# Optimization experiments

Measured on AMD Instinct MI355X. Metric: run time of the kernel, lower is better.

## Reference

```python
import jax, jax.numpy as jnp
import numpy as np

EMBED_DIM = 1024
NUM_HEADS = 16
HEAD_DIM = EMBED_DIM // NUM_HEADS


def setup_inputs() -> dict:
    key = jax.random.key(0)
    ks = jax.random.split(key, 5)
    scale = 1.0 / np.sqrt(EMBED_DIM)
    x = jax.random.normal(ks[0], (2, 2048, EMBED_DIM), dtype=jnp.float32)
    W_qkv = jax.random.uniform(ks[1], (EMBED_DIM, 3 * EMBED_DIM), jnp.float32, -scale, scale)
    b_qkv = jax.random.uniform(ks[2], (3 * EMBED_DIM,), jnp.float32, -scale, scale)
    W_out = jax.random.uniform(ks[3], (EMBED_DIM, EMBED_DIM), jnp.float32, -scale, scale)
    b_out = jax.random.uniform(ks[4], (EMBED_DIM,), jnp.float32, -scale, scale)
    return {"x": x, "W_qkv": W_qkv, "b_qkv": b_qkv, "W_out": W_out, "b_out": b_out}


def reference(x, W_qkv, b_qkv, W_out, b_out):
    B, T, C = x.shape
    H, D = NUM_HEADS, HEAD_DIM
    qkv = x @ W_qkv + b_qkv                       # [B,T,3C]
    q, k, v = jnp.split(qkv, 3, axis=-1)
    # [B,T,C] -> [B,H,T,D]
    q = q.reshape(B, T, H, D).transpose(0, 2, 1, 3)
    k = k.reshape(B, T, H, D).transpose(0, 2, 1, 3)
    v = v.reshape(B, T, H, D).transpose(0, 2, 1, 3)
    scores = jnp.einsum('bhqd,bhkd->bhqk', q, k) / np.sqrt(D)
    attn = jax.nn.softmax(scores, axis=-1)
    out = jnp.einsum('bhqk,bhkd->bhqd', attn, v)  # [B,H,T,D]
    out = out.transpose(0, 2, 1, 3).reshape(B, T, C)
    return out @ W_out + b_out
```

## Files before the change

kernel.cpp:

```cpp
#include <hip/hip_runtime.h>
#include <hip/hip_bf16.h>

#define TB 2048
#define CC 1024
#define HH 16
#define DD 64
#define MM 4096
#define N3 3072
#define KVB 128
#define NT (TB / KVB)

typedef __bf16 bf16x8 __attribute__((ext_vector_type(8)));
typedef float f32x4 __attribute__((ext_vector_type(4)));
typedef float f32x16 __attribute__((ext_vector_type(16)));
typedef unsigned short ushort8 __attribute__((ext_vector_type(8)));
typedef unsigned short u16;

#define QSCALE 0.180336880693612f

__device__ __forceinline__ u16 f2b(float f) {
    unsigned int x = __float_as_uint(f);
    x = (x + 0x7fffu + ((x >> 16) & 1u)) >> 16;
    return (u16)x;
}

__device__ __forceinline__ unsigned cvt_pk_bf16(float lo, float hi) {
    unsigned r;
    asm("v_cvt_pk_bf16_f32 %0, %1, %2" : "=v"(r) : "v"(lo), "v"(hi));
    return r;
}

__device__ __forceinline__ void gld16(const u16* g, u16* l) {
    __builtin_amdgcn_global_load_lds(
        (const __attribute__((address_space(1))) unsigned int*)g,
        (__attribute__((address_space(3))) unsigned int*)l, 16, 0, 0);
}

__global__ __launch_bounds__(256) void prep(const float* __restrict__ x,
                                            u16* __restrict__ xb,
                                            const float* __restrict__ wqkv,
                                            u16* __restrict__ wqkvT,
                                            const float* __restrict__ wout,
                                            u16* __restrict__ woutT) {
    __shared__ float tl[64][65];
    const int bx = blockIdx.x;
    const int tid = threadIdx.x;
    if (bx < 4096) {
        int i = (bx * 256 + tid) * 4;
        float4 v = *reinterpret_cast<const float4*>(x + i);
        union { u16 u[4]; uint2 v2; } r;
        r.u[0] = f2b(v.x); r.u[1] = f2b(v.y); r.u[2] = f2b(v.z); r.u[3] = f2b(v.w);
        *reinterpret_cast<uint2*>(xb + i) = r.v2;
        return;
    }
    const int idx = bx - 4096;
    const int nb = idx & 63, kb = idx >> 6;
    const float* in; u16* out; int N, n0;
    if (nb < 48) { in = wqkv; out = wqkvT; N = 3072; n0 = nb * 64; }
    else         { in = wout; out = woutT; N = 1024; n0 = (nb - 48) * 64; }
    const int k0 = kb * 64;
#pragma unroll
    for (int rep = 0; rep < 4; ++rep) {
        int r = rep * 16 + (tid >> 4);
        int c4 = (tid & 15) * 4;
        float4 v = *reinterpret_cast<const float4*>(&in[(size_t)(k0 + r) * N + n0 + c4]);
        tl[r][c4] = v.x; tl[r][c4 + 1] = v.y; tl[r][c4 + 2] = v.z; tl[r][c4 + 3] = v.w;
    }
    __syncthreads();
#pragma unroll
    for (int rep = 0; rep < 4; ++rep) {
        int nn = rep * 16 + (tid >> 4);
        int kk4 = (tid & 15) * 4;
        union { u16 u[4]; unsigned long long ll; } pk;
#pragma unroll
        for (int i = 0; i < 4; ++i)
            pk.u[i] = f2b(tl[kk4 + i][nn]);
        *reinterpret_cast<unsigned long long*>(&out[(size_t)(n0 + nn) * 1024 + k0 + kk4]) = pk.ll;
    }
}

__global__ __launch_bounds__(512, 2) void gemm_qkv(const u16* __restrict__ xb,
                                                   const u16* __restrict__ wT,
                                                   const float* __restrict__ bias,
                                                   u16* __restrict__ qg,
                                                   u16* __restrict__ kg,
                                                   u16* __restrict__ vtg) {
    __shared__ u16 smem[65536];
    u16* const A0 = smem;
    u16* const B0 = smem + 16384;
    u16* const A1 = smem + 32768;
    u16* const B1 = smem + 49152;
    const int id = blockIdx.y * 12 + blockIdx.x;
    const int xcd = id & 7, pos = id >> 3;
    const int m0 = ((xcd >> 1) * 4 + pos / 6) * 256;
    const int n0 = ((xcd & 1) * 6 + pos % 6) * 256;
    const int tid = threadIdx.x;
    const int w = tid >> 6, lane = tid & 63, lr = lane & 15, h = lane >> 4;
    const int wr = w >> 2, wc = w & 3;
    f32x4 acc[8][4] = {};
    bf16x8 bB[4][2];
    bf16x8 a[2][2];

#define STAGE_SIDE(dstb, srcp, rowbase, kt) do {                                      \
    _Pragma("unroll")                                                                 \
    for (int jj = 0; jj < 4; ++jj) {                                                  \
        int L = jj * 512 + tid;                                                       \
        int rr = L >> 3, c8 = L & 7;                                                  \
        gld16((srcp) + (size_t)((rowbase) + rr) * 1024 + (kt) * 64                    \
                  + ((c8 ^ (rr & 7)) << 3),                                           \
              (dstb) + L * 8);                                                        \
    } } while (0)
#define DSREAD_B(PB) do {                                                             \
    _Pragma("unroll")                                                                 \
    for (int n = 0; n < 4; ++n) {                                                     \
        int R = wc * 64 + n * 16 + lr;                                                \
        const char* br = (const char*)(PB) + R * 128;                                 \
        bB[n][0] = *reinterpret_cast<const bf16x8*>(br + ((h ^ (R & 7)) << 4));       \
        bB[n][1] = *reinterpret_cast<const bf16x8*>(br + (((4 + h) ^ (R & 7)) << 4)); \
    } } while (0)
#define DSREAD_A(PA, mb) do {                                                         \
    _Pragma("unroll")                                                                 \
    for (int mi = 0; mi < 2; ++mi) {                                                  \
        int R = wr * 128 + ((mb) + mi) * 16 + lr;                                     \
        const char* ar = (const char*)(PA) + R * 128;                                 \
        a[mi][0] = *reinterpret_cast<const bf16x8*>(ar + ((h ^ (R & 7)) << 4));       \
        a[mi][1] = *reinterpret_cast<const bf16x8*>(ar + (((4 + h) ^ (R & 7)) << 4)); \
    } } while (0)
#define MFMAP(mb) do {                                                                \
    _Pragma("unroll")                                                                 \
    for (int mi = 0; mi < 2; ++mi)                                                    \
        _Pragma("unroll")                                                             \
        for (int n = 0; n < 4; ++n) {                                                 \
            acc[(mb) + mi][n] = __builtin_amdgcn_mfma_f32_16x16x32_bf16(              \
                a[mi][0], bB[n][0], acc[(mb) + mi][n], 0, 0, 0);                      \
            acc[(mb) + mi][n] = __builtin_amdgcn_mfma_f32_16x16x32_bf16(              \
                a[mi][1], bB[n][1], acc[(mb) + mi][n], 0, 0, 0);                      \
        } } while (0)
#define GBAR __builtin_amdgcn_s_barrier()
#define VMC(n) asm volatile("s_waitcnt vmcnt(" #n ")" ::: "memory")
#define LGK0 do { asm volatile("s_waitcnt lgkmcnt(0)" ::: "memory");                  \
                  __builtin_amdgcn_sched_barrier(0); } while (0)
#define PRI1 __builtin_amdgcn_s_setprio(1)
#define PRI0 __builtin_amdgcn_s_setprio(0)

    STAGE_SIDE(A0, xb, m0, 0);
    STAGE_SIDE(B0, wT, n0, 0);

#pragma unroll 1
    for (int i = 0; i < 7; ++i) {
        const int t1 = 2 * i + 1, t2 = 2 * i + 2;
        STAGE_SIDE(A1, xb, m0, t1);
        VMC(4); GBAR;
        DSREAD_B(B0); DSREAD_A(A0, 0); LGK0;
        PRI1; MFMAP(0); PRI0; GBAR;
        STAGE_SIDE(B1, wT, n0, t1);
        DSREAD_A(A0, 2); GBAR; LGK0; PRI1; MFMAP(2); PRI0; GBAR;
        DSREAD_A(A0, 4); GBAR; LGK0; PRI1; MFMAP(4); PRI0; GBAR;
        DSREAD_A(A0, 6); GBAR; LGK0; PRI1; MFMAP(6); PRI0; GBAR;
        STAGE_SIDE(A0, xb, m0, t2);
        VMC(4); GBAR;
        DSREAD_B(B1); DSREAD_A(A1, 0); LGK0;
        PRI1; MFMAP(0); PRI0; GBAR;
        STAGE_SIDE(B0, wT, n0, t2);
        DSREAD_A(A1, 2); GBAR; LGK0; PRI1; MFMAP(2); PRI0; GBAR;
        DSREAD_A(A1, 4); GBAR; LGK0; PRI1; MFMAP(4); PRI0; GBAR;
        DSREAD_A(A1, 6); GBAR; LGK0; PRI1; MFMAP(6); PRI0; GBAR;
    }
    STAGE_SIDE(A1, xb, m0, 15);
    VMC(4); GBAR;
    DSREAD_B(B0); DSREAD_A(A0, 0); LGK0;
    PRI1; MFMAP(0); PRI0; GBAR;
    STAGE_SIDE(B1, wT, n0, 15);
    DSREAD_A(A0, 2); GBAR; LGK0; PRI1; MFMAP(2); PRI0; GBAR;
    DSREAD_A(A0, 4); GBAR; LGK0; PRI1; MFMAP(4); PRI0; GBAR;
    DSREAD_A(A0, 6); GBAR; LGK0; PRI1; MFMAP(6); PRI0; GBAR;
    VMC(0); GBAR;
    DSREAD_B(B1); DSREAD_A(A1, 0); LGK0;
    PRI1; MFMAP(0); PRI0; GBAR;
    DSREAD_A(A1, 2); GBAR; LGK0; PRI1; MFMAP(2); PRI0; GBAR;
    DSREAD_A(A1, 4); GBAR; LGK0; PRI1; MFMAP(4); PRI0; GBAR;
    DSREAD_A(A1, 6); GBAR; LGK0; PRI1; MFMAP(6); PRI0; GBAR;

#undef STAGE_SIDE
#undef DSREAD_B
#undef DSREAD_A
#undef MFMAP
#undef GBAR
#undef VMC
#undef LGK0
#undef PRI1
#undef PRI0

    const int nthird = n0 >> 10;
    const int b = m0 >> 11, t0 = m0 & 2047;
    float bv[4];
#pragma unroll
    for (int n = 0; n < 4; ++n)
        bv[n] = bias[n0 + wc * 64 + n * 16 + lr];

    __syncthreads();
    if (nthird == 2) {
#pragma unroll
        for (int n = 0; n < 4; ++n) {
            int nloc = wc * 64 + n * 16 + lr;
#pragma unroll
            for (int m = 0; m < 8; ++m) {
                int mloc = wr * 128 + m * 16 + h * 4;
                int mpb = (mloc & ~15) | ((mloc & 4) << 1) | ((mloc & 8) >> 1);
                union { u16 u[4]; unsigned long long ll; } pk4;
#pragma unroll
                for (int reg = 0; reg < 4; ++reg)
                    pk4.u[reg] = f2b(acc[m][n][reg] + bv[n]);
                int slot = mpb >> 3;
                *reinterpret_cast<unsigned long long*>(
                    (char*)smem + nloc * 512 + (((slot ^ (nloc & 31)) << 4) | ((mpb & 7) * 2))) = pk4.ll;
            }
        }
        __syncthreads();
#pragma unroll
        for (int pass = 0; pass < 16; ++pass) {
            int cid = pass * 512 + tid;
            int r = cid >> 5, p = cid & 31;
            ushort8 vch = *reinterpret_cast<const ushort8*>((const char*)smem + r * 512 + (p << 4));
            int tb = p ^ (r & 31);
            int c1 = (n0 & 1023) + r;
            int hh = c1 >> 6, dd = c1 & 63;
            *reinterpret_cast<ushort8*>(
                vtg + ((size_t)(b * HH + hh) * DD + dd) * TB + t0 + tb * 8) = vch;
        }
    } else {
        const float qs = (nthird == 0) ? QSCALE : 1.0f;
#pragma unroll
        for (int m = 0; m < 8; ++m) {
            int rb = wr * 128 + m * 16 + h * 4;
#pragma unroll
            for (int n = 0; n < 4; ++n) {
                int c = wc * 64 + n * 16 + lr;
#pragma unroll
                for (int reg = 0; reg < 4; ++reg) {
                    int r = rb + reg;
                    *reinterpret_cast<u16*>((char*)smem + r * 512 +
                        ((((c >> 3) ^ (r & 31)) << 4) | ((c & 7) << 1)))
                        = f2b((acc[m][n][reg] + bv[n]) * qs);
                }
            }
        }
        __syncthreads();
        u16* dst = (nthird == 0) ? qg : kg;
#pragma unroll
        for (int pass = 0; pass < 16; ++pass) {
            int cid = pass * 512 + tid;
            int r = cid >> 5, p = cid & 31;
            ushort8 vch = *reinterpret_cast<const ushort8*>((const char*)smem + r * 512 + (p << 4));
            int cb = p ^ (r & 31);
            int c1 = (n0 & 1023) + cb * 8;
            int hh = c1 >> 6, dd = c1 & 63;
            *reinterpret_cast<ushort8*>(
                dst + ((size_t)(b * HH + hh) * TB + t0 + r) * DD + dd) = vch;
        }
    }
}

__global__ __launch_bounds__(256, 2) void attn(const u16* __restrict__ qg,
                                               const u16* __restrict__ kg,
                                               const u16* __restrict__ vtg,
                                               u16* __restrict__ ao) {
    __shared__ u16 Kt[2][KVB * 64];
    __shared__ u16 Vt[2][64 * KVB];
    const int bh = blockIdx.x;
    const int q0 = blockIdx.y * 128;
    const int tid = threadIdx.x, w = tid >> 6, lane = tid & 63;
    const int ln = lane & 31, H = lane >> 5;
    const u16* qb = qg + (size_t)bh * TB * DD;
    const u16* kb = kg + (size_t)bh * TB * DD;
    const u16* vb = vtg + (size_t)bh * DD * TB;

#define STAGE(buf, kp, vp) do {                                                         \
    _Pragma("unroll")                                                                   \
    for (int j = 0; j < 4; ++j) {                                                       \
        int L = j * 256 + tid;                                                          \
        int rk = L >> 3, ck = L & 7;                                                    \
        gld16((kp) + (size_t)rk * DD + ((ck ^ (rk & 7)) << 3), Kt[buf] + L * 8);        \
        int rv = L >> 4, cv = L & 15;                                                   \
        gld16((vp) + (size_t)rv * TB + ((cv ^ (rv & 15)) << 3), Vt[buf] + L * 8);       \
    } } while (0)

    bf16x8 bq[4];
#pragma unroll
    for (int dc = 0; dc < 4; ++dc)
        bq[dc] = *reinterpret_cast<const bf16x8*>(
            qb + (size_t)(q0 + w * 32 + ln) * DD + dc * 16 + H * 8);

    f32x16 o[2] = {};
    float m_r = -1e30f;
    float l_r = 0.f;
    f32x16 zero16 = {};

    auto tile_body = [&](const u16* ktc, const u16* vtc) {
        f32x16 s[4];
        __builtin_amdgcn_s_setprio(1);
#pragma unroll
        for (int kb4 = 0; kb4 < 4; ++kb4) {
            int R = kb4 * 32 + ln;
            const char* krow = (const char*)ktc + R * 128;
#pragma unroll
            for (int dc = 0; dc < 4; ++dc) {
                bf16x8 ak = *reinterpret_cast<const bf16x8*>(
                    krow + (((dc * 2 + H) ^ (R & 7)) << 4));
                s[kb4] = __builtin_amdgcn_mfma_f32_32x32x16_bf16(
                    ak, bq[dc], dc == 0 ? zero16 : s[kb4], 0, 0, 0);
            }
        }
        __builtin_amdgcn_s_setprio(0);

        float pm = s[0][0];
#pragma unroll
        for (int kb4 = 0; kb4 < 4; ++kb4) {
            float t0 = fmaxf(fmaxf(s[kb4][0], s[kb4][1]), fmaxf(s[kb4][2], s[kb4][3]));
            float t1 = fmaxf(fmaxf(s[kb4][4], s[kb4][5]), fmaxf(s[kb4][6], s[kb4][7]));
            float t2 = fmaxf(fmaxf(s[kb4][8], s[kb4][9]), fmaxf(s[kb4][10], s[kb4][11]));
            float t3 = fmaxf(fmaxf(s[kb4][12], s[kb4][13]), fmaxf(s[kb4][14], s[kb4][15]));
            pm = fmaxf(pm, fmaxf(fmaxf(t0, t1), fmaxf(t2, t3)));
        }
        pm = fmaxf(pm, __shfl_xor(pm, 32));

        if (!__all(pm - m_r <= 8.0f)) {
            float mn = fmaxf(m_r, pm);
            float fr = __builtin_amdgcn_exp2f(m_r - mn);
            m_r = mn;
            l_r *= fr;
#pragma unroll
            for (int ngd = 0; ngd < 2; ++ngd)
#pragma unroll
                for (int r = 0; r < 16; ++r)
                    o[ngd][r] *= fr;
        }

        float sum = 0.f;
#pragma unroll
        for (int kb4 = 0; kb4 < 4; ++kb4) {
            float ps = 0.f;
#pragma unroll
            for (int r = 0; r < 16; ++r) {
                s[kb4][r] = __builtin_amdgcn_exp2f(s[kb4][r] - m_r);
                ps += s[kb4][r];
            }
            sum += ps;
        }
        sum += __shfl_xor(sum, 32);
        l_r += sum;

        __builtin_amdgcn_s_setprio(1);
#pragma unroll
        for (int kb4 = 0; kb4 < 4; ++kb4) {
#pragma unroll
            for (int b1 = 0; b1 < 2; ++b1) {
                union { unsigned u[4]; bf16x8 v; } ap;
                ap.u[0] = cvt_pk_bf16(s[kb4][8 * b1 + 0], s[kb4][8 * b1 + 1]);
                ap.u[1] = cvt_pk_bf16(s[kb4][8 * b1 + 2], s[kb4][8 * b1 + 3]);
                ap.u[2] = cvt_pk_bf16(s[kb4][8 * b1 + 4], s[kb4][8 * b1 + 5]);
                ap.u[3] = cvt_pk_bf16(s[kb4][8 * b1 + 6], s[kb4][8 * b1 + 7]);
                int c = kb4 * 2 + b1;
#pragma unroll
                for (int ngd = 0; ngd < 2; ++ngd) {
                    int d = ngd * 32 + ln;
                    bf16x8 av = *reinterpret_cast<const bf16x8*>(
                        (const char*)vtc + d * 256 + (((c * 2 + H) ^ (d & 15)) << 4));
                    o[ngd] = __builtin_amdgcn_mfma_f32_32x32x16_bf16(av, ap.v, o[ngd], 0, 0, 0);
                }
            }
        }
        __builtin_amdgcn_s_setprio(0);
    };

    STAGE(0, kb, vb);
    const u16* kp = kb + KVB * DD;
    const u16* vp = vb + KVB;
    __syncthreads();

#pragma unroll 1
    for (int kt2 = 0; kt2 < NT / 2; ++kt2) {
        STAGE(1, kp, vp);
        kp += KVB * DD; vp += KVB;
        tile_body(Kt[0], Vt[0]);
        __syncthreads();
        if (kt2 < NT / 2 - 1) {
            STAGE(0, kp, vp);
            kp += KVB * DD; vp += KVB;
        }
        tile_body(Kt[1], Vt[1]);
        __syncthreads();
    }
#undef STAGE

    const float linv = 1.0f / l_r;
    const int b = bh >> 4, hh = bh & 15;
    const int q = q0 + w * 32 + ln;
    u16* aorow = ao + (size_t)(b * TB + q) * CC + hh * 64;
#pragma unroll
    for (int ngd = 0; ngd < 2; ++ngd) {
#pragma unroll
        for (int rg = 0; rg < 4; ++rg) {
            int dbase = ngd * 32 + 8 * rg + 4 * H;
            union { u16 u[4]; unsigned long long ll; } pk;
#pragma unroll
            for (int r2 = 0; r2 < 4; ++r2)
                pk.u[r2] = f2b(o[ngd][4 * rg + r2] * linv);
            *reinterpret_cast<unsigned long long*>(aorow + dbase) = pk.ll;
        }
    }
}

__global__ __launch_bounds__(256) void gemm_out(const u16* __restrict__ ao,
                                                const u16* __restrict__ wT,
                                                const float* __restrict__ bias,
                                                float* __restrict__ out) {
    __shared__ u16 As[2][64 * 64];
    __shared__ u16 Bs[2][128 * 64];
    const int id = blockIdx.y * 8 + blockIdx.x;
    const int xcd = id & 7, pos = id >> 3;
    const int xr = xcd >> 1, xc = xcd & 1;
    const int pr = pos >> 2, pc = pos & 3;
    const int m0 = (xr * 16 + pr) * 64;
    const int n0 = (xc * 4 + pc) * 128;
    const int tid = threadIdx.x;
    const int w = tid >> 6, lane = tid & 63, lr = lane & 15, h = lane >> 4;
    f32x4 acc[4][2] = {};

#define GO_STAGE(buf, kt) do {                                                        \
    _Pragma("unroll")                                                                 \
    for (int j = 0; j < 2; ++j) {                                                     \
        int L = j * 256 + tid;                                                        \
        int r = L >> 3, c = L & 7;                                                    \
        gld16(ao + (size_t)(m0 + r) * 1024 + (kt) * 64 + ((c ^ (r & 7)) << 3),        \
              As[buf] + L * 8);                                                       \
    }                                                                                 \
    _Pragma("unroll")                                                                 \
    for (int j = 0; j < 4; ++j) {                                                     \
        int L = j * 256 + tid;                                                        \
        int r = L >> 3, c = L & 7;                                                    \
        gld16(wT + (size_t)(n0 + r) * 1024 + (kt) * 64 + ((c ^ (r & 7)) << 3),        \
              Bs[buf] + L * 8);                                                       \
    } } while (0)

    GO_STAGE(0, 0);
    int cur = 0;
#pragma unroll 1
    for (int kt = 0; kt < 16; ++kt) {
        if (kt < 15) {
            GO_STAGE(cur ^ 1, kt + 1);
            asm volatile("s_waitcnt vmcnt(6)" ::: "memory");
        } else {
            asm volatile("s_waitcnt vmcnt(0)" ::: "memory");
        }
        __builtin_amdgcn_s_barrier();
#pragma unroll
        for (int kk = 0; kk < 2; ++kk) {
            bf16x8 a[4], b[2];
            int cc = kk * 4 + h;
#pragma unroll
            for (int m = 0; m < 4; ++m) {
                int R = m * 16 + lr;
                a[m] = *reinterpret_cast<const bf16x8*>((const char*)As[cur] + R * 128 + ((cc ^ (R & 7)) << 4));
            }
#pragma unroll
            for (int n = 0; n < 2; ++n) {
                int R = w * 32 + n * 16 + lr;
                b[n] = *reinterpret_cast<const bf16x8*>((const char*)Bs[cur] + R * 128 + ((cc ^ (R & 7)) << 4));
            }
            __builtin_amdgcn_s_setprio(1);
#pragma unroll
            for (int m = 0; m < 4; ++m)
#pragma unroll
                for (int n = 0; n < 2; ++n)
                    acc[m][n] = __builtin_amdgcn_mfma_f32_16x16x32_bf16(a[m], b[n], acc[m][n], 0, 0, 0);
            __builtin_amdgcn_s_setprio(0);
        }
        __builtin_amdgcn_sched_barrier(0);
        __builtin_amdgcn_s_barrier();
        cur ^= 1;
    }
#undef GO_STAGE

#pragma unroll
    for (int n = 0; n < 2; ++n) {
        int ng = n0 + w * 32 + n * 16 + lr;
        float bv = bias[ng];
#pragma unroll
        for (int m = 0; m < 4; ++m) {
#pragma unroll
            for (int reg = 0; reg < 4; ++reg) {
                int mg = m0 + m * 16 + h * 4 + reg;
                out[(size_t)mg * 1024 + ng] = acc[m][n][reg] + bv;
            }
        }
    }
}

extern "C" void kernel_launch(void* const* d_in, const int* in_sizes, int n_in,
                              void* d_out, int out_size, void* d_ws, size_t ws_size,
                              hipStream_t stream) {
    const float* x     = (const float*)d_in[0];
    const float* W_qkv = (const float*)d_in[1];
    const float* b_qkv = (const float*)d_in[2];
    const float* W_out = (const float*)d_in[3];
    const float* b_out = (const float*)d_in[4];
    float* out = (float*)d_out;

    char* ws = (char*)d_ws;
    u16* xb    = (u16*)(ws);
    u16* wqkvT = (u16*)(ws + (size_t)( 8u << 20));
    u16* woutT = (u16*)(ws + (size_t)(14u << 20));
    u16* qg    = (u16*)(ws + (size_t)(16u << 20));
    u16* kg    = (u16*)(ws + (size_t)(24u << 20));
    u16* vtg   = (u16*)(ws + (size_t)(32u << 20));
    u16* ao    = xb;

    hipLaunchKernelGGL(prep, dim3(5120), dim3(256), 0, stream, x, xb, W_qkv, wqkvT, W_out, woutT);
    hipLaunchKernelGGL(gemm_qkv, dim3(12, 16), dim3(512), 0, stream, xb, wqkvT, b_qkv, qg, kg, vtg);
    hipLaunchKernelGGL(attn, dim3(32, 16), dim3(256), 0, stream, qg, kg, vtg, ao);
    hipLaunchKernelGGL(gemm_out, dim3(8, 64), dim3(256), 0, stream, ao, woutT, b_out, out);
}
```

Before: 110.3 us.

## Software-pipeline attention loop: overlap next tile's QK^T with current softmax+PV

Restructures the attention KV loop so the QK^T MFMAs for tile t+1 are issued before the softmax and PV of tile t, with K and V staged separately at different pipeline offsets. The goal is to let MFMA work overlap with the exp/max VALU work inside one wave and to hide load latency. In exchange it keeps two score accumulators live (sA and sB, 128 extra fp32 registers), which risks spills or lower occupancy under launch_bounds(256,2).

```diff
diff --git a/kernel.cpp b/kernel.cpp
--- a/kernel.cpp
+++ b/kernel.cpp
@@ -275,15 +275,99 @@
     const u16* kb = kg + (size_t)bh * TB * DD;
     const u16* vb = vtg + (size_t)bh * DD * TB;
 
-#define STAGE(buf, kp, vp) do {                                                         \
+#define STAGE_K(buf, kt) do {                                                           \
     _Pragma("unroll")                                                                   \
     for (int j = 0; j < 4; ++j) {                                                       \
         int L = j * 256 + tid;                                                          \
         int rk = L >> 3, ck = L & 7;                                                    \
-        gld16((kp) + (size_t)rk * DD + ((ck ^ (rk & 7)) << 3), Kt[buf] + L * 8);        \
+        gld16(kb + (size_t)((kt) * KVB + rk) * DD + ((ck ^ (rk & 7)) << 3),             \
+              Kt[buf] + L * 8);                                                         \
+    } } while (0)
+#define STAGE_V(buf, kt) do {                                                           \
+    _Pragma("unroll")                                                                   \
+    for (int j = 0; j < 4; ++j) {                                                       \
+        int L = j * 256 + tid;                                                          \
         int rv = L >> 4, cv = L & 15;                                                   \
-        gld16((vp) + (size_t)rv * TB + ((cv ^ (rv & 15)) << 3), Vt[buf] + L * 8);       \
+        gld16(vb + (size_t)rv * TB + (kt) * KVB + ((cv ^ (rv & 15)) << 3),              \
+              Vt[buf] + L * 8);                                                         \
     } } while (0)
+
+#define QK_PHASE(S, KBUF) do {                                                          \
+    const u16* ktc_ = Kt[KBUF];                                                         \
+    __builtin_amdgcn_s_setprio(1);                                                      \
+    _Pragma("unroll")                                                                   \
+    for (int kb4 = 0; kb4 < 4; ++kb4) {                                                 \
+        int R = kb4 * 32 + ln;                                                          \
+        const char* krow = (const char*)ktc_ + R * 128;                                 \
+        _Pragma("unroll")                                                               \
+        for (int dc = 0; dc < 4; ++dc) {                                                \
+            bf16x8 ak = *reinterpret_cast<const bf16x8*>(                               \
+                krow + (((dc * 2 + H) ^ (R & 7)) << 4));                                \
+            S[kb4] = __builtin_amdgcn_mfma_f32_32x32x16_bf16(                           \
+                ak, bq[dc], dc == 0 ? zero16 : S[kb4], 0, 0, 0);                        \
+        }                                                                               \
+    }                                                                                   \
+    __builtin_amdgcn_s_setprio(0);                                                      \
+} while (0)
+
+#define SMPV(S, VBUF) do {                                                              \
+    const u16* vtc_ = Vt[VBUF];                                                         \
+    float pm = S[0][0];                                                                 \
+    _Pragma("unroll")                                                                   \
+    for (int kb4 = 0; kb4 < 4; ++kb4) {                                                 \
+        float t0_ = fmaxf(fmaxf(S[kb4][0], S[kb4][1]), fmaxf(S[kb4][2], S[kb4][3]));    \
+        float t1_ = fmaxf(fmaxf(S[kb4][4], S[kb4][5]), fmaxf(S[kb4][6], S[kb4][7]));    \
+        float t2_ = fmaxf(fmaxf(S[kb4][8], S[kb4][9]), fmaxf(S[kb4][10], S[kb4][11]));  \
+        float t3_ = fmaxf(fmaxf(S[kb4][12], S[kb4][13]), fmaxf(S[kb4][14], S[kb4][15]));\
+        pm = fmaxf(pm, fmaxf(fmaxf(t0_, t1_), fmaxf(t2_, t3_)));                        \
+    }                                                                                   \
+    pm = fmaxf(pm, __shfl_xor(pm, 32));                                                 \
+    if (!__all(pm - m_r <= 8.0f)) {                                                     \
+        float mn = fmaxf(m_r, pm);                                                      \
+        float fr = __builtin_amdgcn_exp2f(m_r - mn);                                    \
+        m_r = mn;                                                                       \
+        l_r *= fr;                                                                      \
+        _Pragma("unroll")                                                               \
+        for (int ngd = 0; ngd < 2; ++ngd)                                               \
+            _Pragma("unroll")                                                           \
+            for (int r = 0; r < 16; ++r)                                                \
+                o[ngd][r] *= fr;                                                        \
+    }                                                                                   \
+    float sum = 0.f;                                                                    \
+    _Pragma("unroll")                                                                   \
+    for (int kb4 = 0; kb4 < 4; ++kb4) {                                                 \
+        float ps = 0.f;                                                                 \
+        _Pragma("unroll")                                                               \
+        for (int r = 0; r < 16; ++r) {                                                  \
+            S[kb4][r] = __builtin_amdgcn_exp2f(S[kb4][r] - m_r);                        \
+            ps += S[kb4][r];                                                            \
+        }                                                                               \
+        sum += ps;                                                                      \
+    }                                                                                   \
+    sum += __shfl_xor(sum, 32);                                                         \
+    l_r += sum;                                                                         \
+    __builtin_amdgcn_s_setprio(1);                                                      \
+    _Pragma("unroll")                                                                   \
+    for (int kb4 = 0; kb4 < 4; ++kb4) {                                                 \
+        _Pragma("unroll")                                                               \
+        for (int b1 = 0; b1 < 2; ++b1) {                                                \
+            union { unsigned u[4]; bf16x8 v; } ap;                                      \
+            ap.u[0] = cvt_pk_bf16(S[kb4][8 * b1 + 0], S[kb4][8 * b1 + 1]);              \
+            ap.u[1] = cvt_pk_bf16(S[kb4][8 * b1 + 2], S[kb4][8 * b1 + 3]);              \
+            ap.u[2] = cvt_pk_bf16(S[kb4][8 * b1 + 4], S[kb4][8 * b1 + 5]);              \
+            ap.u[3] = cvt_pk_bf16(S[kb4][8 * b1 + 6], S[kb4][8 * b1 + 7]);              \
+            int c = kb4 * 2 + b1;                                                       \
+            _Pragma("unroll")                                                           \
+            for (int ngd = 0; ngd < 2; ++ngd) {                                         \
+                int d = ngd * 32 + ln;                                                  \
+                bf16x8 av = *reinterpret_cast<const bf16x8*>(                           \
+                    (const char*)vtc_ + d * 256 + (((c * 2 + H) ^ (d & 15)) << 4));     \
+                o[ngd] = __builtin_amdgcn_mfma_f32_32x32x16_bf16(av, ap.v, o[ngd], 0, 0, 0); \
+            }                                                                           \
+        }                                                                               \
+    }                                                                                   \
+    __builtin_amdgcn_s_setprio(0);                                                      \
+} while (0)
 
     bf16x8 bq[4];
 #pragma unroll
@@ -295,103 +379,39 @@
     float m_r = -1e30f;
     float l_r = 0.f;
     f32x16 zero16 = {};
-
-    auto tile_body = [&](const u16* ktc, const u16* vtc) {
-        f32x16 s[4];
-        __builtin_amdgcn_s_setprio(1);
-#pragma unroll
-        for (int kb4 = 0; kb4 < 4; ++kb4) {
-            int R = kb4 * 32 + ln;
-            const char* krow = (const char*)ktc + R * 128;
-#pragma unroll
-            for (int dc = 0; dc < 4; ++dc) {
-                bf16x8 ak = *reinterpret_cast<const bf16x8*>(
-                    krow + (((dc * 2 + H) ^ (R & 7)) << 4));
-                s[kb4] = __builtin_amdgcn_mfma_f32_32x32x16_bf16(
-                    ak, bq[dc], dc == 0 ? zero16 : s[kb4], 0, 0, 0);
-            }
-        }
-        __builtin_amdgcn_s_setprio(0);
-
-        float pm = s[0][0];
-#pragma unroll
-        for (int kb4 = 0; kb4 < 4; ++kb4) {
-            float t0 = fmaxf(fmaxf(s[kb4][0], s[kb4][1]), fmaxf(s[kb4][2], s[kb4][3]));
-            float t1 = fmaxf(fmaxf(s[kb4][4], s[kb4][5]), fmaxf(s[kb4][6], s[kb4][7]));
-            float t2 = fmaxf(fmaxf(s[kb4][8], s[kb4][9]), fmaxf(s[kb4][10], s[kb4][11]));
-            float t3 = fmaxf(fmaxf(s[kb4][12], s[kb4][13]), fmaxf(s[kb4][14], s[kb4][15]));
-            pm = fmaxf(pm, fmaxf(fmaxf(t0, t1), fmaxf(t2, t3)));
-        }
-        pm = fmaxf(pm, __shfl_xor(pm, 32));
-
-        if (!__all(pm - m_r <= 8.0f)) {
-            float mn = fmaxf(m_r, pm);
-            float fr = __builtin_amdgcn_exp2f(m_r - mn);
-            m_r = mn;
-            l_r *= fr;
-#pragma unroll
-            for (int ngd = 0; ngd < 2; ++ngd)
-#pragma unroll
-                for (int r = 0; r < 16; ++r)
-                    o[ngd][r] *= fr;
-        }
-
-        float sum = 0.f;
-#pragma unroll
-        for (int kb4 = 0; kb4 < 4; ++kb4) {
-            float ps = 0.f;
-#pragma unroll
-            for (int r = 0; r < 16; ++r) {
-                s[kb4][r] = __builtin_amdgcn_exp2f(s[kb4][r] - m_r);
-                ps += s[kb4][r];
-            }
-            sum += ps;
-        }
-        sum += __shfl_xor(sum, 32);
-        l_r += sum;
-
-        __builtin_amdgcn_s_setprio(1);
-#pragma unroll
-        for (int kb4 = 0; kb4 < 4; ++kb4) {
-#pragma unroll
-            for (int b1 = 0; b1 < 2; ++b1) {
-                union { unsigned u[4]; bf16x8 v; } ap;
-                ap.u[0] = cvt_pk_bf16(s[kb4][8 * b1 + 0], s[kb4][8 * b1 + 1]);
-                ap.u[1] = cvt_pk_bf16(s[kb4][8 * b1 + 2], s[kb4][8 * b1 + 3]);
-                ap.u[2] = cvt_pk_bf16(s[kb4][8 * b1 + 4], s[kb4][8 * b1 + 5]);
-                ap.u[3] = cvt_pk_bf16(s[kb4][8 * b1 + 6], s[kb4][8 * b1 + 7]);
-                int c = kb4 * 2 + b1;
-#pragma unroll
-                for (int ngd = 0; ngd < 2; ++ngd) {
-                    int d = ngd * 32 + ln;
-                    bf16x8 av = *reinterpret_cast<const bf16x8*>(
-                        (const char*)vtc + d * 256 + (((c * 2 + H) ^ (d & 15)) << 4));
-                    o[ngd] = __builtin_amdgcn_mfma_f32_32x32x16_bf16(av, ap.v, o[ngd], 0, 0, 0);
-                }
-            }
-        }
-        __builtin_amdgcn_s_setprio(0);
-    };
-
-    STAGE(0, kb, vb);
-    const u16* kp = kb + KVB * DD;
-    const u16* vp = vb + KVB;
+    f32x16 sA[4], sB[4];
+
+    STAGE_K(0, 0);
+    STAGE_V(0, 0);
+    STAGE_K(1, 1);
     __syncthreads();
+    QK_PHASE(sA, 0);
+    __syncthreads();
 
 #pragma unroll 1
-    for (int kt2 = 0; kt2 < NT / 2; ++kt2) {
-        STAGE(1, kp, vp);
-        kp += KVB * DD; vp += KVB;
-        tile_body(Kt[0], Vt[0]);
+    for (int u = 0; u < 7; ++u) {
+        const int t = 2 * u;
+        STAGE_V(1, t + 1);
+        STAGE_K(0, t + 2);
+        QK_PHASE(sB, 1);
+        SMPV(sA, 0);
         __syncthreads();
-        if (kt2 < NT / 2 - 1) {
-            STAGE(0, kp, vp);
-            kp += KVB * DD; vp += KVB;
-        }
-        tile_body(Kt[1], Vt[1]);
+        STAGE_V(0, t + 2);
+        STAGE_K(1, t + 3);
+        QK_PHASE(sA, 0);
+        SMPV(sB, 1);
         __syncthreads();
     }
-#undef STAGE
+    STAGE_V(1, 15);
+    QK_PHASE(sB, 1);
+    SMPV(sA, 0);
+    __syncthreads();
+    SMPV(sB, 1);
+
+#undef STAGE_K
+#undef STAGE_V
+#undef QK_PHASE
+#undef SMPV
 
     const float linv = 1.0f / l_r;
     const int b = bh >> 4, hh = bh & 15;
```

New measurement: 112.2 us. Within noise of the previous version (+1.7%).
